# Optimization experiments

Measured on AMD Instinct MI355X. Metric: run time of the kernel, lower is better.

The kernel has to match this reference:

```python
import jax, jax.numpy as jnp
import numpy as np

D_MODEL = 2048
NUM_HEADS = 32
NUM_KV_GROUPS = 8
D_K = D_MODEL // NUM_HEADS  # 64
KV_DIM = D_K * NUM_KV_GROUPS  # 512
B, S = 2, 2048


def setup_inputs() -> dict:
    key = jax.random.key(0)
    ks = jax.random.split(key, 9)
    sd = 1.0 / np.sqrt(D_MODEL).astype(np.float32)
    return {
        "x": jax.random.normal(ks[0], (B, S, D_MODEL), jnp.float32),
        "wq": jax.random.normal(ks[1], (D_MODEL, D_MODEL), jnp.float32) * sd,
        "bq": jnp.zeros((D_MODEL,), jnp.float32),
        "wk": jax.random.normal(ks[2], (D_MODEL, KV_DIM), jnp.float32) * sd,
        "bk": jnp.zeros((KV_DIM,), jnp.float32),
        "wv": jax.random.normal(ks[3], (D_MODEL, KV_DIM), jnp.float32) * sd,
        "bv": jnp.zeros((KV_DIM,), jnp.float32),
        "wo": jax.random.normal(ks[4], (D_MODEL, D_MODEL), jnp.float32) * sd,
        "bo": jnp.zeros((D_MODEL,), jnp.float32),
    }


def reference(x, wq, bq, wk, bk, wv, bv, wo, bo):
    b, s, _ = x.shape
    # projections (torch Linear = x @ W^T + b; weights here stored as (in,out))
    Q = (x @ wq + bq).reshape(b, s, NUM_HEADS, D_K).transpose(0, 2, 1, 3)       # [B,H,S,dk]
    K = (x @ wk + bk).reshape(b, s, NUM_KV_GROUPS, D_K).transpose(0, 2, 1, 3)   # [B,G,S,dk]
    V = (x @ wv + bv).reshape(b, s, NUM_KV_GROUPS, D_K).transpose(0, 2, 1, 3)   # [B,G,S,dk]
    kv_repeat = NUM_HEADS // NUM_KV_GROUPS
    K_rep = jnp.repeat(K, kv_repeat, axis=1)  # [B,H,S,dk]
    V_rep = jnp.repeat(V, kv_repeat, axis=1)  # [B,H,S,dk]
    scale = 1.0 / jnp.sqrt(jnp.asarray(D_K, x.dtype))
    attn_scores = jnp.einsum("bhqd,bhkd->bhqk", Q, K_rep) * scale
    attn_weights = jax.nn.softmax(attn_scores, axis=-1)                          # [B,H,S,S]
    context = jnp.einsum("bhqk,bhkd->bhqd", attn_weights, V_rep)
    context = context.transpose(0, 2, 1, 3).reshape(b, s, D_MODEL)
    return context @ wo + bo
```

## Files before the change

### kernel.cpp

```cpp
#include <hip/hip_runtime.h>
#include <hip/hip_bf16.h>

typedef __bf16 v8bf16 __attribute__((ext_vector_type(8)));
typedef __bf16 bf16x4 __attribute__((ext_vector_type(4)));
typedef float  f32x4  __attribute__((ext_vector_type(4)));

#define D_MODEL 2048
#define S_LEN   2048
#define NHEADS  32
#define NGROUPS 8
#define DK      64
#define NTOK    4096
#define NQKV    3072
#define QSCALE  0.18033688011112042f

__device__ __forceinline__ void lds_load16(const void* g, void* l) {
  __builtin_amdgcn_global_load_lds(
      (__attribute__((address_space(1))) unsigned int*)g,
      (__attribute__((address_space(3))) unsigned int*)l, 16, 0, 0);
}

__device__ __forceinline__ int sw64(int row, int col) {
  return row * 64 + (col ^ ((row & 7) << 3));
}

__global__ __launch_bounds__(256)
void cvt_f32_bf16(const float* __restrict__ in, __bf16* __restrict__ out, int n) {
  int i = (blockIdx.x * 256 + threadIdx.x) * 4;
  if (i >= n) return;
  float4 v = *(const float4*)(in + i);
  bf16x4 o = { (__bf16)v.x, (__bf16)v.y, (__bf16)v.z, (__bf16)v.w };
  *(bf16x4*)(out + i) = o;
}

__global__ __launch_bounds__(256)
void transpose_cvt(const float* __restrict__ in, __bf16* __restrict__ out, int R, int C) {
  __shared__ float tile[32][33];
  int tx = threadIdx.x, ty = threadIdx.y;
  int c0 = blockIdx.x * 32, r0 = blockIdx.y * 32;
#pragma unroll
  for (int j = 0; j < 4; j++)
    tile[ty + 8 * j][tx] = in[(size_t)(r0 + ty + 8 * j) * C + c0 + tx];
  __syncthreads();
#pragma unroll
  for (int j = 0; j < 4; j++)
    out[(size_t)(c0 + ty + 8 * j) * R + r0 + tx] = (__bf16)tile[tx][ty + 8 * j];
}

__global__ __launch_bounds__(256)
void transpose_bf16(const __bf16* __restrict__ in, __bf16* __restrict__ out,
                    int R, int C, int ldin, int ldout) {
  __shared__ __bf16 tile[32][33];
  int tx = threadIdx.x, ty = threadIdx.y;
  int c0 = blockIdx.x * 32, r0 = blockIdx.y * 32;
#pragma unroll
  for (int j = 0; j < 4; j++)
    tile[ty + 8 * j][tx] = in[(size_t)(r0 + ty + 8 * j) * ldin + c0 + tx];
  __syncthreads();
#pragma unroll
  for (int j = 0; j < 4; j++)
    out[(size_t)(c0 + ty + 8 * j) * ldout + r0 + tx] = tile[tx][ty + 8 * j];
}

template <int MODE, int BN>
__global__ __launch_bounds__(512, 1)
void gemm_big(const __bf16* __restrict__ A, const __bf16* __restrict__ BT,
              const float* __restrict__ b0, const float* __restrict__ b1,
              const float* __restrict__ b2,
              __bf16* __restrict__ Cb, float* __restrict__ Cf,
              int M, int N, int K) {
  constexpr int FN = BN / 64;
  __shared__ __bf16 Alds[2 * 256 * 64];
  __shared__ __bf16 Blds[3 * BN * 64];
  const int t = threadIdx.x;
  const int lane = t & 63, w = t >> 6;
  const int lr = lane & 15, lg = lane >> 4;
  const int wm = w >> 2, wn = w & 3;
  const int cpx = gridDim.x >> 3;
  const int swz = (blockIdx.x & 7) * cpx + (blockIdx.x >> 3);
  const int nbx = N / BN;
  const int m0 = (swz / nbx) * 256, n0 = (swz % nbx) * BN;
  const int scol = (((t & 7) ^ ((t >> 3) & 7)) << 3);

  const __bf16* Abase = A + (size_t)(m0 + (t >> 3)) * K + scol;
  const __bf16* Bbase = BT + (size_t)(n0 + (t >> 3)) * K + scol;

  auto stageA = [&](int tile, int c) {
    lds_load16(Abase + (size_t)(c * 64) * K + tile * 64,
               Alds + (tile & 1) * 16384 + c * 4096 + t * 8);
  };
  auto stageB = [&](int tile, int bi, int c) {
    lds_load16(Bbase + (size_t)(c * 64) * K + tile * 64,
               Blds + bi * (BN * 64) + c * 4096 + t * 8);
  };

  const f32x4 fz = {0.f, 0.f, 0.f, 0.f};
  f32x4 acc[8][FN];
#pragma unroll
  for (int fm = 0; fm < 8; fm++)
#pragma unroll
    for (int fn = 0; fn < FN; fn++) acc[fm][fn] = fz;

#pragma unroll
  for (int c = 0; c < 4; c++) stageA(0, c);
#pragma unroll
  for (int c = 0; c < FN; c++) stageB(0, 0, c);
  stageA(1, 0);
  stageA(1, 2);
#pragma unroll
  for (int c = 0; c < FN; c++) stageB(1, 1, c);

  int bcur = 0, bn1 = 1, bn2 = 2;
  for (int kt = 0; kt < 32; kt++) {
    if (kt < 31) {
      if constexpr (FN == 3) asm volatile("s_waitcnt vmcnt(5)" ::: "memory");
      else                   asm volatile("s_waitcnt vmcnt(4)" ::: "memory");
    } else {
      asm volatile("s_waitcnt vmcnt(0)" ::: "memory");
    }
    __builtin_amdgcn_s_barrier();
    __builtin_amdgcn_sched_barrier(0);

    const __bf16* Ab = Alds + (kt & 1) * 16384;
    const __bf16* Bb = Blds + bcur * (BN * 64);
    v8bf16 bfr[2][FN];

    {
#pragma unroll
      for (int fn = 0; fn < FN; fn++)
        bfr[0][fn] = *(const v8bf16*)&Bb[sw64(wn * (BN / 4) + fn * 16 + lr, lg * 8)];
      v8bf16 af[4];
#pragma unroll
      for (int j = 0; j < 4; j++)
        af[j] = *(const v8bf16*)&Ab[sw64(wm * 128 + j * 16 + lr, lg * 8)];
      if (kt < 31) stageA(kt + 1, 1);
      __builtin_amdgcn_s_barrier();
      __builtin_amdgcn_sched_barrier(0);
      __builtin_amdgcn_s_setprio(1);
#pragma unroll
      for (int j = 0; j < 4; j++)
#pragma unroll
        for (int fn = 0; fn < FN; fn++)
          acc[j][fn] = __builtin_amdgcn_mfma_f32_16x16x32_bf16(af[j], bfr[0][fn], acc[j][fn], 0, 0, 0);
      __builtin_amdgcn_s_setprio(0);
      __builtin_amdgcn_sched_barrier(0);
      __builtin_amdgcn_s_barrier();
    }
    {
#pragma unroll
      for (int fn = 0; fn < FN; fn++)
        bfr[1][fn] = *(const v8bf16*)&Bb[sw64(wn * (BN / 4) + fn * 16 + lr, 32 + lg * 8)];
      v8bf16 af[4];
#pragma unroll
      for (int j = 0; j < 4; j++)
        af[j] = *(const v8bf16*)&Ab[sw64(wm * 128 + j * 16 + lr, 32 + lg * 8)];
      if (kt < 31) stageA(kt + 1, 3);
      __builtin_amdgcn_s_barrier();
      __builtin_amdgcn_sched_barrier(0);
      __builtin_amdgcn_s_setprio(1);
#pragma unroll
      for (int j = 0; j < 4; j++)
#pragma unroll
        for (int fn = 0; fn < FN; fn++)
          acc[j][fn] = __builtin_amdgcn_mfma_f32_16x16x32_bf16(af[j], bfr[1][fn], acc[j][fn], 0, 0, 0);
      __builtin_amdgcn_s_setprio(0);
      __builtin_amdgcn_sched_barrier(0);
      __builtin_amdgcn_s_barrier();
    }
    {
      v8bf16 af[4];
#pragma unroll
      for (int j = 0; j < 4; j++)
        af[j] = *(const v8bf16*)&Ab[sw64(wm * 128 + 64 + j * 16 + lr, lg * 8)];
      if (kt < 30) { stageA(kt + 2, 0); stageB(kt + 2, bn2, 0); }
      __builtin_amdgcn_s_barrier();
      __builtin_amdgcn_sched_barrier(0);
      __builtin_amdgcn_s_setprio(1);
#pragma unroll
      for (int j = 0; j < 4; j++)
#pragma unroll
        for (int fn = 0; fn < FN; fn++)
          acc[4 + j][fn] = __builtin_amdgcn_mfma_f32_16x16x32_bf16(af[j], bfr[0][fn], acc[4 + j][fn], 0, 0, 0);
      __builtin_amdgcn_s_setprio(0);
      __builtin_amdgcn_sched_barrier(0);
      __builtin_amdgcn_s_barrier();
    }
    {
      v8bf16 af[4];
#pragma unroll
      for (int j = 0; j < 4; j++)
        af[j] = *(const v8bf16*)&Ab[sw64(wm * 128 + 64 + j * 16 + lr, 32 + lg * 8)];
      if (kt < 30) {
        stageA(kt + 2, 2);
        stageB(kt + 2, bn2, 1);
        if constexpr (FN == 3) stageB(kt + 2, bn2, 2);
      }
      __builtin_amdgcn_s_barrier();
      __builtin_amdgcn_sched_barrier(0);
      __builtin_amdgcn_s_setprio(1);
#pragma unroll
      for (int j = 0; j < 4; j++)
#pragma unroll
        for (int fn = 0; fn < FN; fn++)
          acc[4 + j][fn] = __builtin_amdgcn_mfma_f32_16x16x32_bf16(af[j], bfr[1][fn], acc[4 + j][fn], 0, 0, 0);
      __builtin_amdgcn_s_setprio(0);
      __builtin_amdgcn_sched_barrier(0);
    }

    int tmp = bcur; bcur = bn1; bn1 = bn2; bn2 = tmp;
  }

#pragma unroll
  for (int fn = 0; fn < FN; fn++) {
    int col = n0 + wn * (BN / 4) + fn * 16 + lr;
    float bias, scale = 1.0f;
    if (MODE == 0) {
      if (col < 2048)      { bias = b0[col];        scale = QSCALE; }
      else if (col < 2560) { bias = b1[col - 2048]; }
      else                 { bias = b2[col - 2560]; }
    } else {
      bias = b0[col];
    }
#pragma unroll
    for (int fm = 0; fm < 8; fm++)
#pragma unroll
      for (int r = 0; r < 4; r++) {
        int row = m0 + wm * 128 + fm * 16 + lg * 4 + r;
        float v = acc[fm][fn][r] + bias;
        if (MODE == 0) Cb[(size_t)row * N + col] = (__bf16)(v * scale);
        else           Cf[(size_t)row * N + col] = v;
      }
  }
}

__global__ __launch_bounds__(512, 2)
void attn_kernel(const __bf16* __restrict__ QKV, const __bf16* __restrict__ VT,
                 __bf16* __restrict__ ctx) {
  __shared__ __bf16 smem[26624];
  const int t = threadIdx.x;
  const int lane = t & 63, w = t >> 6;
  const int lr = lane & 15, lg = lane >> 4;
  const int flat = blockIdx.y * 8 + blockIdx.x;
  const int swz = (flat & 7) * 64 + (flat >> 3);
  const int qt = swz & 7, bh = swz >> 3;
  const int b = bh >> 5, h = bh & 31, g = h >> 2;
  const int q0 = qt * 256;
  const int scol = (((t & 7) ^ ((t >> 3) & 7)) << 3);

  v8bf16 qa[2][2];
#pragma unroll
  for (int mi = 0; mi < 2; mi++)
#pragma unroll
    for (int dk2 = 0; dk2 < 2; dk2++)
      qa[mi][dk2] = *(const v8bf16*)(QKV +
          (size_t)(b * S_LEN + q0 + w * 32 + mi * 16 + lr) * NQKV + h * DK + dk2 * 32 + lg * 8);

  const __bf16* kp = QKV + (size_t)(b * S_LEN + (t >> 3)) * NQKV + D_MODEL + g * DK + scol;
  const __bf16* vp = VT + (size_t)(g * DK + (t >> 3)) * NTOK + b * S_LEN + scol;

  lds_load16(kp, smem + t * 8);
  lds_load16(vp, smem + 4096 + t * 8);
  __syncthreads();

  const int kloff0 = lr * 64 + ((lg * 8) ^ ((lr & 7) << 3));
  const int kloff1 = lr * 64 + ((32 + lg * 8) ^ ((lr & 7) << 3));
  __bf16* Pw = smem + 16384 + w * 1280;

  const __bf16 one1 = (__bf16)1.0f;
  const v8bf16 ones = { one1, one1, one1, one1, one1, one1, one1, one1 };
  const f32x4 fz = {0.f, 0.f, 0.f, 0.f};
  f32x4 o[2][4], o_sum[2];
  o_sum[0] = fz; o_sum[1] = fz;
#pragma unroll
  for (int mi = 0; mi < 2; mi++)
#pragma unroll
    for (int nd = 0; nd < 4; nd++) o[mi][nd] = fz;

#pragma unroll 2
  for (int kt = 0; kt < 32; kt++) {
    if (kt < 31) {
      __bf16* nb = smem + ((kt & 1) ^ 1) * 8192;
      lds_load16(kp + (size_t)64 * NQKV, nb + t * 8);
      lds_load16(vp + 64, nb + 4096 + t * 8);
      kp += (size_t)64 * NQKV;
      vp += 64;
    }
    const __bf16* Kb = smem + (kt & 1) * 8192;
    const __bf16* k0 = Kb + kloff0;
    const __bf16* k1 = Kb + kloff1;

    f32x4 st[4][2];
#pragma unroll
    for (int ni = 0; ni < 4; ni++) { st[ni][0] = fz; st[ni][1] = fz; }
    __builtin_amdgcn_s_setprio(1);
#pragma unroll
    for (int ni = 0; ni < 4; ni++) {
      v8bf16 kb = *(const v8bf16*)(k0 + ni * 1024);
      st[ni][0] = __builtin_amdgcn_mfma_f32_16x16x32_bf16(kb, qa[0][0], st[ni][0], 0, 0, 0);
      st[ni][1] = __builtin_amdgcn_mfma_f32_16x16x32_bf16(kb, qa[1][0], st[ni][1], 0, 0, 0);
    }
#pragma unroll
    for (int ni = 0; ni < 4; ni++) {
      v8bf16 kb = *(const v8bf16*)(k1 + ni * 1024);
      st[ni][0] = __builtin_amdgcn_mfma_f32_16x16x32_bf16(kb, qa[0][1], st[ni][0], 0, 0, 0);
      st[ni][1] = __builtin_amdgcn_mfma_f32_16x16x32_bf16(kb, qa[1][1], st[ni][1], 0, 0, 0);
    }
    __builtin_amdgcn_s_setprio(0);

#pragma unroll
    for (int ks = 0; ks < 2; ks++) {
      const __bf16* vbase = (ks ? k1 : k0) + 4096;
#pragma unroll
      for (int mi = 0; mi < 2; mi++)
#pragma unroll
        for (int ni2 = 0; ni2 < 2; ni2++) {
          f32x4 sv = st[2 * ks + ni2][mi];
          bf16x4 pk = { (__bf16)exp2f(sv[0]), (__bf16)exp2f(sv[1]),
                        (__bf16)exp2f(sv[2]), (__bf16)exp2f(sv[3]) };
          *(bf16x4*)(Pw + (mi * 16 + lr) * 40 + ni2 * 16 + lg * 4) = pk;
        }
      v8bf16 pa0 = *(const v8bf16*)(Pw + lr * 40 + lg * 8);
      v8bf16 pa1 = *(const v8bf16*)(Pw + (16 + lr) * 40 + lg * 8);
      __builtin_amdgcn_s_setprio(1);
#pragma unroll
      for (int nd = 0; nd < 4; nd++) {
        v8bf16 vb = *(const v8bf16*)(vbase + nd * 1024);
        o[0][nd] = __builtin_amdgcn_mfma_f32_16x16x32_bf16(pa0, vb, o[0][nd], 0, 0, 0);
        o[1][nd] = __builtin_amdgcn_mfma_f32_16x16x32_bf16(pa1, vb, o[1][nd], 0, 0, 0);
      }
      o_sum[0] = __builtin_amdgcn_mfma_f32_16x16x32_bf16(pa0, ones, o_sum[0], 0, 0, 0);
      o_sum[1] = __builtin_amdgcn_mfma_f32_16x16x32_bf16(pa1, ones, o_sum[1], 0, 0, 0);
      __builtin_amdgcn_s_setprio(0);
    }

    __syncthreads();
  }

#pragma unroll
  for (int mi = 0; mi < 2; mi++)
#pragma unroll
    for (int r = 0; r < 4; r++) {
      float inv = 1.0f / o_sum[mi][r];
      int row = b * S_LEN + q0 + w * 32 + mi * 16 + lg * 4 + r;
#pragma unroll
      for (int nd = 0; nd < 4; nd++)
        ctx[(size_t)row * D_MODEL + h * DK + nd * 16 + lr] = (__bf16)(o[mi][nd][r] * inv);
    }
}

extern "C" void kernel_launch(void* const* d_in, const int* in_sizes, int n_in,
                              void* d_out, int out_size, void* d_ws, size_t ws_size,
                              hipStream_t stream) {
  (void)in_sizes; (void)n_in; (void)out_size; (void)ws_size;
  const float* x  = (const float*)d_in[0];
  const float* wq = (const float*)d_in[1];
  const float* bq = (const float*)d_in[2];
  const float* wk = (const float*)d_in[3];
  const float* bk = (const float*)d_in[4];
  const float* wv = (const float*)d_in[5];
  const float* bv = (const float*)d_in[6];
  const float* wo = (const float*)d_in[7];
  const float* bo = (const float*)d_in[8];

  char* ws = (char*)d_ws;
  __bf16* xb    = (__bf16*)(ws);
  __bf16* wqkvT = (__bf16*)(ws + 16777216);
  __bf16* woT   = (__bf16*)(ws + 29360128);
  __bf16* QKVb  = (__bf16*)(ws + 37748736);
  __bf16* VbT   = (__bf16*)(ws + 62914560);
  __bf16* ctx   = (__bf16*)(ws + 67108864);

  dim3 tb(32, 8);
  cvt_f32_bf16<<<8192, 256, 0, stream>>>(x, xb, NTOK * D_MODEL);
  transpose_cvt<<<dim3(64, 64), tb, 0, stream>>>(wq, wqkvT, 2048, 2048);
  transpose_cvt<<<dim3(16, 64), tb, 0, stream>>>(wk, wqkvT + 2048 * 2048, 2048, 512);
  transpose_cvt<<<dim3(16, 64), tb, 0, stream>>>(wv, wqkvT + 2560 * 2048, 2048, 512);
  transpose_cvt<<<dim3(64, 64), tb, 0, stream>>>(wo, woT, 2048, 2048);

  gemm_big<0, 192><<<dim3(256), 512, 0, stream>>>(xb, wqkvT, bq, bk, bv,
                                                  QKVb, nullptr, NTOK, NQKV, 2048);
  transpose_bf16<<<dim3(16, 128), tb, 0, stream>>>(QKVb + 2560, VbT, 4096, 512, 3072, 4096);
  attn_kernel<<<dim3(8, 64), 512, 0, stream>>>(QKVb, VbT, ctx);
  gemm_big<1, 128><<<dim3(256), 512, 0, stream>>>(ctx, woT, bo, nullptr, nullptr,
                                                  nullptr, (float*)d_out, NTOK, 2048, 2048);
}
```

Measured before the change: 223.2 us.

## Load V fragments directly from global into registers and merge weight transposes

```diff
diff --git a/kernel.cpp b/kernel.cpp
--- a/kernel.cpp
+++ b/kernel.cpp
@@ -34,9 +34,20 @@
 }
 
 __global__ __launch_bounds__(256)
-void transpose_cvt(const float* __restrict__ in, __bf16* __restrict__ out, int R, int C) {
+void transpose_cvt_all(const float* __restrict__ wq, const float* __restrict__ wk,
+                       const float* __restrict__ wv, const float* __restrict__ wo,
+                       __bf16* __restrict__ wqkvT, __bf16* __restrict__ woT) {
   __shared__ float tile[32][33];
-  int tx = threadIdx.x, ty = threadIdx.y;
+  const int tx = threadIdx.x, ty = threadIdx.y;
+  const float* in;
+  __bf16* out;
+  int C;
+  const int z = blockIdx.z;
+  if (z == 0)      { in = wq; out = wqkvT;              C = 2048; }
+  else if (z == 1) { if (blockIdx.x >= 16) return; in = wk; out = wqkvT + 2048 * 2048; C = 512; }
+  else if (z == 2) { if (blockIdx.x >= 16) return; in = wv; out = wqkvT + 2560 * 2048; C = 512; }
+  else             { in = wo; out = woT;                C = 2048; }
+  const int R = 2048;
   int c0 = blockIdx.x * 32, r0 = blockIdx.y * 32;
 #pragma unroll
   for (int j = 0; j < 4; j++)
@@ -233,10 +244,10 @@
   }
 }
 
-__global__ __launch_bounds__(512, 2)
+__global__ __launch_bounds__(512, 4)
 void attn_kernel(const __bf16* __restrict__ QKV, const __bf16* __restrict__ VT,
                  __bf16* __restrict__ ctx) {
-  __shared__ __bf16 smem[26624];
+  __shared__ __bf16 smem[18432];
   const int t = threadIdx.x;
   const int lane = t & 63, w = t >> 6;
   const int lr = lane & 15, lg = lane >> 4;
@@ -256,15 +267,14 @@
           (size_t)(b * S_LEN + q0 + w * 32 + mi * 16 + lr) * NQKV + h * DK + dk2 * 32 + lg * 8);
 
   const __bf16* kp = QKV + (size_t)(b * S_LEN + (t >> 3)) * NQKV + D_MODEL + g * DK + scol;
-  const __bf16* vp = VT + (size_t)(g * DK + (t >> 3)) * NTOK + b * S_LEN + scol;
+  const __bf16* vgp = VT + (size_t)(g * DK + lr) * NTOK + b * S_LEN + lg * 8;
 
   lds_load16(kp, smem + t * 8);
-  lds_load16(vp, smem + 4096 + t * 8);
   __syncthreads();
 
   const int kloff0 = lr * 64 + ((lg * 8) ^ ((lr & 7) << 3));
   const int kloff1 = lr * 64 + ((32 + lg * 8) ^ ((lr & 7) << 3));
-  __bf16* Pw = smem + 16384 + w * 1280;
+  __bf16* Pw = smem + 8192 + w * 1280;
 
   const __bf16 one1 = (__bf16)1.0f;
   const v8bf16 ones = { one1, one1, one1, one1, one1, one1, one1, one1 };
@@ -279,13 +289,15 @@
 #pragma unroll 2
   for (int kt = 0; kt < 32; kt++) {
     if (kt < 31) {
-      __bf16* nb = smem + ((kt & 1) ^ 1) * 8192;
-      lds_load16(kp + (size_t)64 * NQKV, nb + t * 8);
-      lds_load16(vp + 64, nb + 4096 + t * 8);
+      lds_load16(kp + (size_t)64 * NQKV, smem + (((kt & 1) ^ 1) << 12) + t * 8);
       kp += (size_t)64 * NQKV;
-      vp += 64;
-    }
-    const __bf16* Kb = smem + (kt & 1) * 8192;
+    }
+    v8bf16 vb0[4], vb1[4];
+#pragma unroll
+    for (int nd = 0; nd < 4; nd++)
+      vb0[nd] = *(const v8bf16*)(vgp + nd * 16 * NTOK);
+
+    const __bf16* Kb = smem + ((kt & 1) << 12);
     const __bf16* k0 = Kb + kloff0;
     const __bf16* k1 = Kb + kloff1;
 
@@ -306,10 +318,13 @@
       st[ni][1] = __builtin_amdgcn_mfma_f32_16x16x32_bf16(kb, qa[1][1], st[ni][1], 0, 0, 0);
     }
     __builtin_amdgcn_s_setprio(0);
+#pragma unroll
+    for (int nd = 0; nd < 4; nd++)
+      vb1[nd] = *(const v8bf16*)(vgp + nd * 16 * NTOK + 32);
+    vgp += 64;
 
 #pragma unroll
     for (int ks = 0; ks < 2; ks++) {
-      const __bf16* vbase = (ks ? k1 : k0) + 4096;
 #pragma unroll
       for (int mi = 0; mi < 2; mi++)
 #pragma unroll
@@ -324,7 +339,7 @@
       __builtin_amdgcn_s_setprio(1);
 #pragma unroll
       for (int nd = 0; nd < 4; nd++) {
-        v8bf16 vb = *(const v8bf16*)(vbase + nd * 1024);
+        v8bf16 vb = ks ? vb1[nd] : vb0[nd];
         o[0][nd] = __builtin_amdgcn_mfma_f32_16x16x32_bf16(pa0, vb, o[0][nd], 0, 0, 0);
         o[1][nd] = __builtin_amdgcn_mfma_f32_16x16x32_bf16(pa1, vb, o[1][nd], 0, 0, 0);
       }
@@ -372,10 +387,7 @@
 
   dim3 tb(32, 8);
   cvt_f32_bf16<<<8192, 256, 0, stream>>>(x, xb, NTOK * D_MODEL);
-  transpose_cvt<<<dim3(64, 64), tb, 0, stream>>>(wq, wqkvT, 2048, 2048);
-  transpose_cvt<<<dim3(16, 64), tb, 0, stream>>>(wk, wqkvT + 2048 * 2048, 2048, 512);
-  transpose_cvt<<<dim3(16, 64), tb, 0, stream>>>(wv, wqkvT + 2560 * 2048, 2048, 512);
-  transpose_cvt<<<dim3(64, 64), tb, 0, stream>>>(wo, woT, 2048, 2048);
+  transpose_cvt_all<<<dim3(64, 64, 4), tb, 0, stream>>>(wq, wk, wv, wo, wqkvT, woT);
 
   gemm_big<0, 192><<<dim3(256), 512, 0, stream>>>(xb, wqkvT, bq, bk, bv,
                                                   QKVb, nullptr, NTOK, NQKV, 2048);
```

Result: slower. 398.0 us (+78.3%).
